# Performance work log

Hardware: AMD Instinct MI355X
Metric: run time of the kernel (lower is better)

The kernel has to match this reference:

```python
import jax, jax.numpy as jnp
import numpy as np

D_MODEL = 1024
N_HEADS = 16
HEAD_DIM = D_MODEL // N_HEADS
D_FF = 4096
LN_EPS = 1e-5


def setup_inputs() -> dict:
    key = jax.random.key(0)
    ks = jax.random.split(key, 13)
    s = lambda fan_in: 1.0 / np.sqrt(fan_in)
    return {
        "x": jax.random.normal(ks[0], (2, 2048, D_MODEL), dtype=jnp.float32),
        "w_qkv": jax.random.uniform(ks[1], (D_MODEL, 3 * D_MODEL), jnp.float32, -s(D_MODEL), s(D_MODEL)),
        "b_qkv": jax.random.uniform(ks[2], (3 * D_MODEL,), jnp.float32, -s(D_MODEL), s(D_MODEL)),
        "w_out": jax.random.uniform(ks[3], (D_MODEL, D_MODEL), jnp.float32, -s(D_MODEL), s(D_MODEL)),
        "b_out": jax.random.uniform(ks[4], (D_MODEL,), jnp.float32, -s(D_MODEL), s(D_MODEL)),
        "w_ff1": jax.random.uniform(ks[5], (D_MODEL, D_FF), jnp.float32, -s(D_MODEL), s(D_MODEL)),
        "b_ff1": jax.random.uniform(ks[6], (D_FF,), jnp.float32, -s(D_MODEL), s(D_MODEL)),
        "w_ff2": jax.random.uniform(ks[7], (D_FF, D_MODEL), jnp.float32, -s(D_FF), s(D_FF)),
        "b_ff2": jax.random.uniform(ks[8], (D_MODEL,), jnp.float32, -s(D_FF), s(D_FF)),
        "ln1_g": jnp.ones((D_MODEL,), jnp.float32),
        "ln1_b": jnp.zeros((D_MODEL,), jnp.float32),
        "ln2_g": jnp.ones((D_MODEL,), jnp.float32),
        "ln2_b": jnp.zeros((D_MODEL,), jnp.float32),
    }


def _layer_norm(x, g, b):
    mu = jnp.mean(x, axis=-1, keepdims=True)
    var = jnp.mean(jnp.square(x - mu), axis=-1, keepdims=True)
    return (x - mu) * jax.lax.rsqrt(var + LN_EPS) * g + b


def reference(x, w_qkv, b_qkv, w_out, b_out, w_ff1, b_ff1, w_ff2, b_ff2,
              ln1_g, ln1_b, ln2_g, ln2_b):
    B, S, D = x.shape
    scale = HEAD_DIM ** -0.5
    qkv = x @ w_qkv + b_qkv                                   # [B,S,3D]
    qkv = qkv.reshape(B, S, 3, N_HEADS, HEAD_DIM)
    q, k, v = (qkv[:, :, 0], qkv[:, :, 1], qkv[:, :, 2])      # [B,S,H,Dh]
    attn = jnp.einsum("bqhd,bkhd->bhqk", q, k) * scale        # [B,H,S,S]
    attn = jax.nn.softmax(attn, axis=-1)
    o = jnp.einsum("bhqk,bkhd->bqhd", attn, v).reshape(B, S, D)
    o = o @ w_out + b_out
    x = _layer_norm(x + o, ln1_g, ln1_b)
    # FFN: Linear -> exact GELU -> Linear (dropout = 0)
    h = jax.nn.gelu(x @ w_ff1 + b_ff1, approximate=False)
    ff = h @ w_ff2 + b_ff2
    x = _layer_norm(x + ff, ln2_g, ln2_b)
    return x
```

## Files before the change

kernel.cpp:

```cpp
#include <hip/hip_runtime.h>
#include <hip/hip_bf16.h>
#include <cstdint>
#include <cstddef>

using bf16 = __hip_bfloat16;
typedef __attribute__((ext_vector_type(8))) short bf16x8;
typedef __attribute__((ext_vector_type(4))) float f32x4;

#define TOKENS 4096
#define DMODEL 1024
#define DFF    4096
#define SEQ    2048
#define NHEAD  16
#define HDIM   64
#define KVBLK  64
#define NT     (SEQ / KVBLK)

__device__ __forceinline__ void async16(const void* g, void* l) {
  __builtin_amdgcn_global_load_lds(
      (const __attribute__((address_space(1))) void*)g,
      (__attribute__((address_space(3))) void*)l, 16, 0, 0);
}

__device__ __forceinline__ f32x4 mfma16(bf16x8 a, bf16x8 b, f32x4 c) {
  return __builtin_amdgcn_mfma_f32_16x16x32_bf16(a, b, c, 0, 0, 0);
}

__global__ void cast_bf16_k(const float* __restrict__ src, bf16* __restrict__ dst, int n) {
  int i = (blockIdx.x * blockDim.x + threadIdx.x) * 4;
  if (i >= n) return;
  float4 v = *(const float4*)(src + i);
  dst[i + 0] = __float2bfloat16(v.x);
  dst[i + 1] = __float2bfloat16(v.y);
  dst[i + 2] = __float2bfloat16(v.z);
  dst[i + 3] = __float2bfloat16(v.w);
}

__global__ void transpose_cast_k(const float* __restrict__ src, bf16* __restrict__ dst,
                                 int K, int N) {
  __shared__ float tile[32][33];
  int nt = blockIdx.x * 32, kt = blockIdx.y * 32;
  int tx = threadIdx.x, ty = threadIdx.y;
  #pragma unroll
  for (int i = 0; i < 32; i += 8)
    tile[ty + i][tx] = src[(size_t)(kt + ty + i) * N + nt + tx];
  __syncthreads();
  #pragma unroll
  for (int i = 0; i < 32; i += 8)
    dst[(size_t)(nt + ty + i) * K + kt + tx] = __float2bfloat16(tile[tx][ty + i]);
}

template <int EPI, int BN>
__global__ __launch_bounds__(256, 2)
void gemm_bt(const bf16* __restrict__ A, const bf16* __restrict__ Bt,
             const float* __restrict__ bias, int M, int N, int K,
             float* __restrict__ outf, bf16* __restrict__ outb,
             const float* __restrict__ resid,
             bf16* __restrict__ Qb, bf16* __restrict__ Kb, bf16* __restrict__ Vtb) {
  constexpr int MR = (BN == 128) ? 4 : 2;
  __shared__ bf16 Al[2][128 * 32];
  __shared__ bf16 Bl[2][BN * 32];
  const int t = threadIdx.x;
  const int nwg = gridDim.x * gridDim.y;
  const int flat = blockIdx.y * gridDim.x + blockIdx.x;
  const int swz = (flat & 7) * (nwg >> 3) + (flat >> 3);
  const int bm = (swz / gridDim.x) * 128, bn = (swz % gridDim.x) * BN;
  const int wid = t >> 6, lane = t & 63, g = lane >> 4, r = lane & 15;
  const int wr = (BN == 128) ? (wid >> 1) * 64 : wid * 32;
  const int wc = (BN == 128) ? (wid & 1) * 64 : 0;

  const f32x4 zero = {0.f, 0.f, 0.f, 0.f};
  f32x4 acc[MR][4];
  #pragma unroll
  for (int i = 0; i < MR; i++)
    #pragma unroll
    for (int j = 0; j < 4; j++) acc[i][j] = zero;

  const int ar0 = t >> 2, ac = (t & 3) * 8;
  const int ar1 = ar0 + 64;
  const int ach0 = t * 16, ach1 = ach0 + 4096;

  const int NK = K >> 5;
  #define STAGE(ktile, pb)                                                          \
    do {                                                                            \
      const int kk = (ktile) << 5;                                                  \
      async16(A + (size_t)(bm + ar0) * K + kk + ac, (char*)Al[pb] + ach0);          \
      async16(A + (size_t)(bm + ar1) * K + kk + ac, (char*)Al[pb] + ach1);          \
      async16(Bt + (size_t)(bn + ar0) * K + kk + ac, (char*)Bl[pb] + ach0);         \
      if constexpr (BN == 128)                                                      \
        async16(Bt + (size_t)(bn + ar1) * K + kk + ac, (char*)Bl[pb] + ach1);       \
    } while (0)

  STAGE(0, 0);
  asm volatile("s_waitcnt vmcnt(0)" ::: "memory");
  __builtin_amdgcn_s_barrier();

  #pragma unroll 1
  for (int it = 0; it < NK; ++it) {
    const int cur = it & 1;
    if (it + 1 < NK) STAGE(it + 1, cur ^ 1);
    bf16x8 af[MR], bfr[4];
    #pragma unroll
    for (int mt = 0; mt < MR; mt++)
      af[mt] = *(const bf16x8*)&Al[cur][(wr + mt * 16 + r) * 32 + 8 * g];
    #pragma unroll
    for (int nt = 0; nt < 4; nt++)
      bfr[nt] = *(const bf16x8*)&Bl[cur][(wc + nt * 16 + r) * 32 + 8 * g];
    #pragma unroll
    for (int mt = 0; mt < MR; mt++)
      #pragma unroll
      for (int nt = 0; nt < 4; nt++)
        acc[mt][nt] = mfma16(af[mt], bfr[nt], acc[mt][nt]);
    __builtin_amdgcn_sched_barrier(0);
    asm volatile("s_waitcnt vmcnt(0)" ::: "memory");
    __builtin_amdgcn_s_barrier();
  }
  #undef STAGE

  #pragma unroll
  for (int nt = 0; nt < 4; nt++) {
    const int col = bn + wc + nt * 16 + r;
    const float bv = bias[col];
    #pragma unroll
    for (int mt = 0; mt < MR; mt++) {
      #pragma unroll
      for (int j = 0; j < 4; j++) {
        const int row = bm + wr + mt * 16 + 4 * g + j;
        float v = acc[mt][nt][j] + bv;
        if constexpr (EPI == 0) {
          const int part = col >> 10, hd = col & 1023, h = hd >> 6, d = hd & 63;
          const int b_ = row >> 11, s_ = row & 2047;
          const bf16 q = __float2bfloat16(v);
          if (part == 0)      Qb[((size_t)(b_ * NHEAD + h) * SEQ + s_) * HDIM + d] = q;
          else if (part == 1) Kb[((size_t)(b_ * NHEAD + h) * SEQ + s_) * HDIM + d] = q;
          else                Vtb[((size_t)(b_ * NHEAD + h) * HDIM + d) * SEQ + s_] = q;
        } else if constexpr (EPI == 1) {
          const size_t idx = (size_t)row * N + col;
          outf[idx] = v + resid[idx];
        } else {
          const size_t idx = (size_t)row * N + col;
          outb[idx] = __float2bfloat16(0.5f * v * (1.f + erff(v * 0.70710678118f)));
        }
      }
    }
  }
}

__global__ __launch_bounds__(256, 4)
void attn_k(const bf16* __restrict__ Q, const bf16* __restrict__ Km,
            const bf16* __restrict__ Vt, bf16* __restrict__ O) {
  __shared__ bf16 Kl[2][KVBLK * 64];
  __shared__ bf16 Vl[2][KVBLK * 64];
  __shared__ bf16 P[4][16 * 64];
  const int b = blockIdx.x;
  const int bswz = (b & 7) * 128 + (b >> 3);
  const int bh = bswz >> 5, qb = bswz & 31;
  const int t = threadIdx.x, wid = t >> 6, lane = t & 63, g = lane >> 4, r = lane & 15;
  const int q0 = qb * 64 + wid * 16;
  const bf16* Qp = Q + (size_t)bh * SEQ * HDIM;
  const char* Kc = (const char*)(Km + (size_t)bh * SEQ * HDIM);
  const char* Vc = (const char*)(Vt + (size_t)bh * HDIM * SEQ);

  const bf16x8 qf0 = *(const bf16x8*)&Qp[(q0 + r) * HDIM + 8 * g];
  const bf16x8 qf1 = *(const bf16x8*)&Qp[(q0 + r) * HDIM + 8 * g + 32];

  const int o0 = wid * 2048 + lane * 16, o1 = o0 + 1024;
  const int cs0 = ((((o0 >> 4) & 7) ^ ((o0 >> 7) & 7)) << 4);
  const int cs1 = ((((o1 >> 4) & 7) ^ ((o1 >> 7) & 7)) << 4);
  const int kso0 = (o0 & ~127) + cs0, kso1 = (o1 & ~127) + cs1;
  const int vso0 = (o0 >> 7) * (SEQ * 2) + cs0, vso1 = (o1 >> 7) * (SEQ * 2) + cs1;

  const f32x4 zero = {0.f, 0.f, 0.f, 0.f};
  f32x4 oacc[4];
  #pragma unroll
  for (int i = 0; i < 4; i++) oacc[i] = zero;
  float mrow = -1e30f, lrow = 0.f;
  bf16* pl = P[wid];
  const int cA = ((g ^ (r & 7)) << 3), cB = (((g + 4) ^ (r & 7)) << 3);

  {
    const char* ks = Kc; const char* vs = Vc;
    char* kd = (char*)Kl[0]; char* vd = (char*)Vl[0];
    async16(ks + kso0, kd + o0); async16(ks + kso1, kd + o1);
    async16(vs + vso0, vd + o0); async16(vs + vso1, vd + o1);
  }

  #pragma unroll 1
  for (int tt = 0; tt < NT; ++tt) {
    if (tt + 1 < NT) {
      const char* ks = Kc + (tt + 1) * (KVBLK * HDIM * 2);
      const char* vs = Vc + (tt + 1) * (KVBLK * 2);
      char* kd = (char*)Kl[(tt + 1) & 1]; char* vd = (char*)Vl[(tt + 1) & 1];
      async16(ks + kso0, kd + o0); async16(ks + kso1, kd + o1);
      async16(vs + vso0, vd + o0); async16(vs + vso1, vd + o1);
      asm volatile("s_waitcnt vmcnt(4)" ::: "memory");
    } else {
      asm volatile("s_waitcnt vmcnt(0)" ::: "memory");
    }
    __builtin_amdgcn_sched_barrier(0);
    __builtin_amdgcn_s_barrier();
    __builtin_amdgcn_sched_barrier(0);

    const bf16* kbuf = Kl[tt & 1];
    const bf16* vbuf = Vl[tt & 1];

    f32x4 sacc[4];
    #pragma unroll
    for (int kt = 0; kt < 4; kt++) {
      const bf16* krow = kbuf + (kt * 16 + r) * 64;
      bf16x8 ka = *(const bf16x8*)&krow[cA];
      bf16x8 kb = *(const bf16x8*)&krow[cB];
      f32x4 s = zero;
      s = mfma16(ka, qf0, s);
      s = mfma16(kb, qf1, s);
      sacc[kt] = s;
    }

    float sv[4][4];
    #pragma unroll
    for (int kt = 0; kt < 4; kt++)
      #pragma unroll
      for (int j = 0; j < 4; j++) sv[kt][j] = sacc[kt][j] * 0.125f;
    float m0 = fmaxf(fmaxf(sv[0][0], sv[0][1]), fmaxf(sv[0][2], sv[0][3]));
    float m1 = fmaxf(fmaxf(sv[1][0], sv[1][1]), fmaxf(sv[1][2], sv[1][3]));
    float m2 = fmaxf(fmaxf(sv[2][0], sv[2][1]), fmaxf(sv[2][2], sv[2][3]));
    float m3 = fmaxf(fmaxf(sv[3][0], sv[3][1]), fmaxf(sv[3][2], sv[3][3]));
    float mx = fmaxf(fmaxf(m0, m1), fmaxf(m2, m3));
    mx = fmaxf(mx, __shfl_xor(mx, 16));
    mx = fmaxf(mx, __shfl_xor(mx, 32));
    const float mn = fmaxf(mrow, mx);
    const float corr = __expf(mrow - mn);
    mrow = mn;
    float sum = 0.f;
    #pragma unroll
    for (int kt = 0; kt < 4; kt++)
      #pragma unroll
      for (int j = 0; j < 4; j++) {
        const float p = __expf(sv[kt][j] - mn);
        sv[kt][j] = p;
        sum += p;
      }
    sum += __shfl_xor(sum, 16);
    sum += __shfl_xor(sum, 32);
    lrow = lrow * corr + sum;

    #pragma unroll
    for (int kt = 0; kt < 4; kt++) {
      bf16 pk[4] = {__float2bfloat16(sv[kt][0]), __float2bfloat16(sv[kt][1]),
                    __float2bfloat16(sv[kt][2]), __float2bfloat16(sv[kt][3])};
      const int pc = (((kt * 2 + (g >> 1)) ^ (r & 7)) << 4) + ((g & 1) << 3);
      *(short4*)((char*)pl + r * 128 + pc) = *(const short4*)pk;
    }
    asm volatile("s_waitcnt lgkmcnt(0)" ::: "memory");
    __builtin_amdgcn_sched_barrier(0);
    const bf16x8 pf0 = *(const bf16x8*)((const char*)pl + r * 128 + (cA << 1));
    const bf16x8 pf1 = *(const bf16x8*)((const char*)pl + r * 128 + (cB << 1));

    float cq[4];
    #pragma unroll
    for (int j = 0; j < 4; j++) cq[j] = __shfl(corr, 4 * g + j);

    #pragma unroll
    for (int dt = 0; dt < 4; dt++) {
      const bf16* vrow = vbuf + (dt * 16 + r) * 64;
      bf16x8 v0 = *(const bf16x8*)&vrow[cA];
      bf16x8 v1 = *(const bf16x8*)&vrow[cB];
      #pragma unroll
      for (int j = 0; j < 4; j++) oacc[dt][j] *= cq[j];
      oacc[dt] = mfma16(pf0, v0, oacc[dt]);
      oacc[dt] = mfma16(pf1, v1, oacc[dt]);
    }
    __builtin_amdgcn_sched_barrier(0);
    __builtin_amdgcn_s_barrier();
  }

  float lq[4];
  #pragma unroll
  for (int j = 0; j < 4; j++) lq[j] = __shfl(lrow, 4 * g + j);
  const int b_ = bh >> 4, h = bh & 15;
  #pragma unroll
  for (int dt = 0; dt < 4; dt++)
    #pragma unroll
    for (int j = 0; j < 4; j++) {
      const int tok = b_ * SEQ + q0 + 4 * g + j;
      O[(size_t)tok * DMODEL + h * HDIM + dt * 16 + r] =
          __float2bfloat16(oacc[dt][j] / lq[j]);
    }
}

__global__ __launch_bounds__(256)
void ln_k(const float* __restrict__ in, const float* __restrict__ gw,
          const float* __restrict__ bw, float* __restrict__ outf,
          bf16* __restrict__ outb) {
  const int row = blockIdx.x, t = threadIdx.x;
  const float4 v = *(const float4*)(in + (size_t)row * DMODEL + t * 4);
  float s = v.x + v.y + v.z + v.w;
  float s2 = v.x * v.x + v.y * v.y + v.z * v.z + v.w * v.w;
  #pragma unroll
  for (int m = 1; m < 64; m <<= 1) { s += __shfl_xor(s, m); s2 += __shfl_xor(s2, m); }
  __shared__ float red[8];
  const int wid = t >> 6, lane = t & 63;
  if (lane == 0) { red[wid] = s; red[4 + wid] = s2; }
  __syncthreads();
  s = red[0] + red[1] + red[2] + red[3];
  s2 = red[4] + red[5] + red[6] + red[7];
  const float mu = s * (1.f / DMODEL);
  const float rstd = rsqrtf(s2 * (1.f / DMODEL) - mu * mu + 1e-5f);
  const float4 gv = *(const float4*)(gw + t * 4);
  const float4 bv = *(const float4*)(bw + t * 4);
  float o0 = (v.x - mu) * rstd * gv.x + bv.x;
  float o1 = (v.y - mu) * rstd * gv.y + bv.y;
  float o2 = (v.z - mu) * rstd * gv.z + bv.z;
  float o3 = (v.w - mu) * rstd * gv.w + bv.w;
  if (outf) {
    float4 ov = {o0, o1, o2, o3};
    *(float4*)(outf + (size_t)row * DMODEL + t * 4) = ov;
  }
  if (outb) {
    bf16* p = outb + (size_t)row * DMODEL + t * 4;
    p[0] = __float2bfloat16(o0); p[1] = __float2bfloat16(o1);
    p[2] = __float2bfloat16(o2); p[3] = __float2bfloat16(o3);
  }
}

extern "C" void kernel_launch(void* const* d_in, const int* in_sizes, int n_in,
                              void* d_out, int out_size, void* d_ws, size_t ws_size,
                              hipStream_t stream) {
  const float* x     = (const float*)d_in[0];
  const float* w_qkv = (const float*)d_in[1];
  const float* b_qkv = (const float*)d_in[2];
  const float* w_out = (const float*)d_in[3];
  const float* b_out = (const float*)d_in[4];
  const float* w_ff1 = (const float*)d_in[5];
  const float* b_ff1 = (const float*)d_in[6];
  const float* w_ff2 = (const float*)d_in[7];
  const float* b_ff2 = (const float*)d_in[8];
  const float* ln1_g = (const float*)d_in[9];
  const float* ln1_b = (const float*)d_in[10];
  const float* ln2_g = (const float*)d_in[11];
  const float* ln2_b = (const float*)d_in[12];
  float* out = (float*)d_out;

  char* base = (char*)d_ws;
  bf16* wqkvT = (bf16*)(base);
  bf16* woutT = (bf16*)(base + 6291456);
  bf16* wff1T = (bf16*)(base + 8388608);
  bf16* wff2T = (bf16*)(base + 16777216);
  bf16* Qb    = (bf16*)(base + 25165824);
  bf16* Kb    = (bf16*)(base + 33554432);
  bf16* Vtb   = (bf16*)(base + 41943040);
  bf16* xob   = (bf16*)(base + 50331648);
  bf16* hb    = (bf16*)(base + 25165824);
  float* y    = (float*)(base + 58720256);
  float* x1f  = (float*)(base + 75497472);
  bf16* x1b   = (bf16*)(base + 92274688);
  (void)in_sizes; (void)n_in; (void)out_size; (void)ws_size;

  dim3 tb(32, 8);
  transpose_cast_k<<<dim3(3072 / 32, 1024 / 32), tb, 0, stream>>>(w_qkv, wqkvT, 1024, 3072);
  transpose_cast_k<<<dim3(1024 / 32, 1024 / 32), tb, 0, stream>>>(w_out, woutT, 1024, 1024);
  transpose_cast_k<<<dim3(4096 / 32, 1024 / 32), tb, 0, stream>>>(w_ff1, wff1T, 1024, 4096);
  transpose_cast_k<<<dim3(1024 / 32, 4096 / 32), tb, 0, stream>>>(w_ff2, wff2T, 4096, 1024);
  cast_bf16_k<<<(TOKENS * DMODEL / 4 + 255) / 256, 256, 0, stream>>>(x, xob, TOKENS * DMODEL);

  gemm_bt<0, 128><<<dim3(3072 / 128, TOKENS / 128), 256, 0, stream>>>(
      xob, wqkvT, b_qkv, TOKENS, 3072, 1024, nullptr, nullptr, nullptr, Qb, Kb, Vtb);
  attn_k<<<dim3(1024), 256, 0, stream>>>(Qb, Kb, Vtb, xob);
  gemm_bt<1, 64><<<dim3(1024 / 64, TOKENS / 128), 256, 0, stream>>>(
      xob, woutT, b_out, TOKENS, 1024, 1024, y, nullptr, x, nullptr, nullptr, nullptr);
  ln_k<<<TOKENS, 256, 0, stream>>>(y, ln1_g, ln1_b, x1f, x1b);
  gemm_bt<2, 128><<<dim3(4096 / 128, TOKENS / 128), 256, 0, stream>>>(
      x1b, wff1T, b_ff1, TOKENS, 4096, 1024, nullptr, hb, nullptr, nullptr, nullptr, nullptr);
  gemm_bt<1, 64><<<dim3(1024 / 64, TOKENS / 128), 256, 0, stream>>>(
      hb, wff2T, b_ff2, TOKENS, 1024, 4096, y, nullptr, x1f, nullptr, nullptr, nullptr);
  ln_k<<<TOKENS, 256, 0, stream>>>(y, ln2_g, ln2_b, out, nullptr);
}
```

Before: 290.7 us.

## Add 256x256 GEMM for QKV/FF1, fold softmax scale into Q, lazy rescale

Adds a new 512-thread GEMM kernel with 256x256 tiles, BK=64 and XOR-swizzled LDS, used for the QKV and FF1 projections. The QKV epilogue pre-scales Q by scale*log2(e) so attention can use exp2 directly. Attention now rescales the running max and output accumulator only when the new block max exceeds the old one by more than 8. s_setprio is wrapped around the MFMA sections in every kernel. The larger tiles increase register and LDS pressure and the wave count drops, and lazy rescaling relies on tolerating bounded exponent growth.

Result: slower. 315.5 us (+8.5%).

```diff
diff --git a/kernel.cpp b/kernel.cpp
--- a/kernel.cpp
+++ b/kernel.cpp
@@ -15,6 +15,7 @@
 #define HDIM   64
 #define KVBLK  64
 #define NT     (SEQ / KVBLK)
+#define QSCALE 0.1803368801111f
 
 __device__ __forceinline__ void async16(const void* g, void* l) {
   __builtin_amdgcn_global_load_lds(
@@ -48,6 +49,148 @@
   #pragma unroll
   for (int i = 0; i < 32; i += 8)
     dst[(size_t)(nt + ty + i) * K + kt + tx] = __float2bfloat16(tile[tx][ty + i]);
+}
+
+template <int EPI>
+__global__ __launch_bounds__(512, 2)
+void gemm256(const bf16* __restrict__ A, const bf16* __restrict__ Bt,
+             const float* __restrict__ bias, int M, int N, int K,
+             bf16* __restrict__ outb,
+             bf16* __restrict__ Qb, bf16* __restrict__ Kb, bf16* __restrict__ Vtb) {
+  __shared__ bf16 Al[2][256 * 64];
+  __shared__ bf16 Bl[2][256 * 64];
+  const int t = threadIdx.x;
+  const int nwg = gridDim.x * gridDim.y;
+  const int flat = blockIdx.y * gridDim.x + blockIdx.x;
+  const int swz = (flat & 7) * (nwg >> 3) + (flat >> 3);
+  const int bm = (swz / gridDim.x) * 256, bn = (swz % gridDim.x) * 256;
+  const int lane = t & 63, wid = t >> 6, g = lane >> 4, r = lane & 15;
+  const int wr = (wid >> 2) * 128, wc = (wid & 3) * 64;
+
+  const f32x4 zero = {0.f, 0.f, 0.f, 0.f};
+  f32x4 acc[8][4];
+  #pragma unroll
+  for (int i = 0; i < 8; i++)
+    #pragma unroll
+    for (int j = 0; j < 4; j++) acc[i][j] = zero;
+
+  const int srow = t >> 3, schunk = t & 7;
+  const int scol = ((schunk ^ (srow & 7)) << 3);
+
+  #define STAGE256(ktile, pb)                                             \
+    do {                                                                  \
+      const bf16* As = A + (size_t)(bm + srow) * K + (ktile) * 64 + scol; \
+      const bf16* Bs = Bt + (size_t)(bn + srow) * K + (ktile) * 64 + scol;\
+      char* Ad = (char*)Al[pb] + t * 16;                                  \
+      char* Bd = (char*)Bl[pb] + t * 16;                                  \
+      async16(As,            Ad);                                         \
+      async16(As + 64 * K,   Ad + 8192);                                  \
+      async16(As + 128 * K,  Ad + 16384);                                 \
+      async16(As + 192 * K,  Ad + 24576);                                 \
+      async16(Bs,            Bd);                                         \
+      async16(Bs + 64 * K,   Bd + 8192);                                  \
+      async16(Bs + 128 * K,  Bd + 16384);                                 \
+      async16(Bs + 192 * K,  Bd + 24576);                                 \
+    } while (0)
+
+  STAGE256(0, 0);
+  STAGE256(1, 1);
+  asm volatile("s_waitcnt vmcnt(8)" ::: "memory");
+  __builtin_amdgcn_sched_barrier(0);
+  __builtin_amdgcn_s_barrier();
+  __builtin_amdgcn_sched_barrier(0);
+
+  const int c0 = ((0 * 4 + g) ^ (r & 7)) << 4;
+  const int c1 = ((1 * 4 + g) ^ (r & 7)) << 4;
+
+  const int NK = K >> 6;
+  #pragma unroll 1
+  for (int tt = 0; tt < NK; ++tt) {
+    const int cur = tt & 1;
+    const char* Ab = (const char*)Al[cur];
+    const char* Bb = (const char*)Bl[cur];
+    bf16x8 bfr[4][2], af[4][2];
+    #pragma unroll
+    for (int nt = 0; nt < 4; nt++) {
+      const int rb = (wc + nt * 16 + r) * 128;
+      bfr[nt][0] = *(const bf16x8*)(Bb + rb + c0);
+      bfr[nt][1] = *(const bf16x8*)(Bb + rb + c1);
+    }
+    #pragma unroll
+    for (int mt = 0; mt < 4; mt++) {
+      const int rb = (wr + mt * 16 + r) * 128;
+      af[mt][0] = *(const bf16x8*)(Ab + rb + c0);
+      af[mt][1] = *(const bf16x8*)(Ab + rb + c1);
+    }
+    __builtin_amdgcn_s_setprio(1);
+    #pragma unroll
+    for (int mt = 0; mt < 4; mt++)
+      #pragma unroll
+      for (int nt = 0; nt < 4; nt++) {
+        acc[mt][nt] = mfma16(af[mt][0], bfr[nt][0], acc[mt][nt]);
+        acc[mt][nt] = mfma16(af[mt][1], bfr[nt][1], acc[mt][nt]);
+      }
+    __builtin_amdgcn_s_setprio(0);
+    #pragma unroll
+    for (int mt = 0; mt < 4; mt++) {
+      const int rb = (wr + 64 + mt * 16 + r) * 128;
+      af[mt][0] = *(const bf16x8*)(Ab + rb + c0);
+      af[mt][1] = *(const bf16x8*)(Ab + rb + c1);
+    }
+    __builtin_amdgcn_s_setprio(1);
+    #pragma unroll
+    for (int mt = 0; mt < 4; mt++)
+      #pragma unroll
+      for (int nt = 0; nt < 4; nt++) {
+        acc[4 + mt][nt] = mfma16(af[mt][0], bfr[nt][0], acc[4 + mt][nt]);
+        acc[4 + mt][nt] = mfma16(af[mt][1], bfr[nt][1], acc[4 + mt][nt]);
+      }
+    __builtin_amdgcn_s_setprio(0);
+    if (tt + 1 < NK) {
+      __builtin_amdgcn_sched_barrier(0);
+      __builtin_amdgcn_s_barrier();
+      __builtin_amdgcn_sched_barrier(0);
+      if (tt + 2 < NK) {
+        STAGE256(tt + 2, cur);
+        asm volatile("s_waitcnt vmcnt(8)" ::: "memory");
+      } else {
+        asm volatile("s_waitcnt vmcnt(0)" ::: "memory");
+      }
+      __builtin_amdgcn_sched_barrier(0);
+      __builtin_amdgcn_s_barrier();
+      __builtin_amdgcn_sched_barrier(0);
+    }
+  }
+  #undef STAGE256
+
+  #pragma unroll
+  for (int nt = 0; nt < 4; nt++) {
+    const int col = bn + wc + nt * 16 + r;
+    const float bv = bias[col];
+    #pragma unroll
+    for (int mt = 0; mt < 8; mt++) {
+      #pragma unroll
+      for (int j = 0; j < 4; j++) {
+        const int row = bm + wr + mt * 16 + 4 * g + j;
+        float v = acc[mt][nt][j] + bv;
+        if constexpr (EPI == 0) {
+          const int part = col >> 10, hd = col & 1023, h = hd >> 6, d = hd & 63;
+          const int b_ = row >> 11, s_ = row & 2047;
+          if (part == 0) {
+            Qb[((size_t)(b_ * NHEAD + h) * SEQ + s_) * HDIM + d] =
+                __float2bfloat16(v * QSCALE);
+          } else if (part == 1) {
+            Kb[((size_t)(b_ * NHEAD + h) * SEQ + s_) * HDIM + d] = __float2bfloat16(v);
+          } else {
+            Vtb[((size_t)(b_ * NHEAD + h) * HDIM + d) * SEQ + s_] = __float2bfloat16(v);
+          }
+        } else {
+          outb[(size_t)row * N + col] =
+              __float2bfloat16(0.5f * v * (1.f + erff(v * 0.70710678118f)));
+        }
+      }
+    }
+  }
 }
 
 template <int EPI, int BN>
@@ -106,11 +249,13 @@
     #pragma unroll
     for (int nt = 0; nt < 4; nt++)
       bfr[nt] = *(const bf16x8*)&Bl[cur][(wc + nt * 16 + r) * 32 + 8 * g];
+    __builtin_amdgcn_s_setprio(1);
     #pragma unroll
     for (int mt = 0; mt < MR; mt++)
       #pragma unroll
       for (int nt = 0; nt < 4; nt++)
         acc[mt][nt] = mfma16(af[mt], bfr[nt], acc[mt][nt]);
+    __builtin_amdgcn_s_setprio(0);
     __builtin_amdgcn_sched_barrier(0);
     asm volatile("s_waitcnt vmcnt(0)" ::: "memory");
     __builtin_amdgcn_s_barrier();
@@ -127,23 +272,12 @@
       for (int j = 0; j < 4; j++) {
         const int row = bm + wr + mt * 16 + 4 * g + j;
         float v = acc[mt][nt][j] + bv;
-        if constexpr (EPI == 0) {
-          const int part = col >> 10, hd = col & 1023, h = hd >> 6, d = hd & 63;
-          const int b_ = row >> 11, s_ = row & 2047;
-          const bf16 q = __float2bfloat16(v);
-          if (part == 0)      Qb[((size_t)(b_ * NHEAD + h) * SEQ + s_) * HDIM + d] = q;
-          else if (part == 1) Kb[((size_t)(b_ * NHEAD + h) * SEQ + s_) * HDIM + d] = q;
-          else                Vtb[((size_t)(b_ * NHEAD + h) * HDIM + d) * SEQ + s_] = q;
-        } else if constexpr (EPI == 1) {
-          const size_t idx = (size_t)row * N + col;
-          outf[idx] = v + resid[idx];
-        } else {
-          const size_t idx = (size_t)row * N + col;
-          outb[idx] = __float2bfloat16(0.5f * v * (1.f + erff(v * 0.70710678118f)));
-        }
+        const size_t idx = (size_t)row * N + col;
+        outf[idx] = v + resid[idx];
       }
     }
   }
+  (void)outb; (void)Qb; (void)Kb; (void)Vtb;
 }
 
 __global__ __launch_bounds__(256, 4)
@@ -179,10 +313,9 @@
   const int cA = ((g ^ (r & 7)) << 3), cB = (((g + 4) ^ (r & 7)) << 3);
 
   {
-    const char* ks = Kc; const char* vs = Vc;
     char* kd = (char*)Kl[0]; char* vd = (char*)Vl[0];
-    async16(ks + kso0, kd + o0); async16(ks + kso1, kd + o1);
-    async16(vs + vso0, vd + o0); async16(vs + vso1, vd + o1);
+    async16(Kc + kso0, kd + o0); async16(Kc + kso1, kd + o1);
+    async16(Vc + vso0, vd + o0); async16(Vc + vso1, vd + o1);
   }
 
   #pragma unroll 1
@@ -205,6 +338,7 @@
     const bf16* vbuf = Vl[tt & 1];
 
     f32x4 sacc[4];
+    __builtin_amdgcn_s_setprio(1);
     #pragma unroll
     for (int kt = 0; kt < 4; kt++) {
       const bf16* krow = kbuf + (kt * 16 + r) * 64;
@@ -215,28 +349,29 @@
       s = mfma16(kb, qf1, s);
       sacc[kt] = s;
     }
-
-    float sv[4][4];
-    #pragma unroll
-    for (int kt = 0; kt < 4; kt++)
-      #pragma unroll
-      for (int j = 0; j < 4; j++) sv[kt][j] = sacc[kt][j] * 0.125f;
-    float m0 = fmaxf(fmaxf(sv[0][0], sv[0][1]), fmaxf(sv[0][2], sv[0][3]));
-    float m1 = fmaxf(fmaxf(sv[1][0], sv[1][1]), fmaxf(sv[1][2], sv[1][3]));
-    float m2 = fmaxf(fmaxf(sv[2][0], sv[2][1]), fmaxf(sv[2][2], sv[2][3]));
-    float m3 = fmaxf(fmaxf(sv[3][0], sv[3][1]), fmaxf(sv[3][2], sv[3][3]));
+    __builtin_amdgcn_s_setprio(0);
+
+    float m0 = fmaxf(fmaxf(sacc[0][0], sacc[0][1]), fmaxf(sacc[0][2], sacc[0][3]));
+    float m1 = fmaxf(fmaxf(sacc[1][0], sacc[1][1]), fmaxf(sacc[1][2], sacc[1][3]));
+    float m2 = fmaxf(fmaxf(sacc[2][0], sacc[2][1]), fmaxf(sacc[2][2], sacc[2][3]));
+    float m3 = fmaxf(fmaxf(sacc[3][0], sacc[3][1]), fmaxf(sacc[3][2], sacc[3][3]));
     float mx = fmaxf(fmaxf(m0, m1), fmaxf(m2, m3));
     mx = fmaxf(mx, __shfl_xor(mx, 16));
     mx = fmaxf(mx, __shfl_xor(mx, 32));
-    const float mn = fmaxf(mrow, mx);
-    const float corr = __expf(mrow - mn);
-    mrow = mn;
+    const bool grow = !__all(mx <= mrow + 8.f);
+    float corr = 1.f;
+    if (grow) {
+      const float mn = fmaxf(mrow, mx);
+      corr = exp2f(mrow - mn);
+      mrow = mn;
+    }
     float sum = 0.f;
+    float sv[4][4];
     #pragma unroll
     for (int kt = 0; kt < 4; kt++)
       #pragma unroll
       for (int j = 0; j < 4; j++) {
-        const float p = __expf(sv[kt][j] - mn);
+        const float p = exp2f(sacc[kt][j] - mrow);
         sv[kt][j] = p;
         sum += p;
       }
@@ -256,20 +391,26 @@
     const bf16x8 pf0 = *(const bf16x8*)((const char*)pl + r * 128 + (cA << 1));
     const bf16x8 pf1 = *(const bf16x8*)((const char*)pl + r * 128 + (cB << 1));
 
-    float cq[4];
-    #pragma unroll
-    for (int j = 0; j < 4; j++) cq[j] = __shfl(corr, 4 * g + j);
-
+    if (grow) {
+      float cq[4];
+      #pragma unroll
+      for (int j = 0; j < 4; j++) cq[j] = __shfl(corr, 4 * g + j);
+      #pragma unroll
+      for (int dt = 0; dt < 4; dt++)
+        #pragma unroll
+        for (int j = 0; j < 4; j++) oacc[dt][j] *= cq[j];
+    }
+
+    __builtin_amdgcn_s_setprio(1);
     #pragma unroll
     for (int dt = 0; dt < 4; dt++) {
       const bf16* vrow = vbuf + (dt * 16 + r) * 64;
       bf16x8 v0 = *(const bf16x8*)&vrow[cA];
       bf16x8 v1 = *(const bf16x8*)&vrow[cB];
-      #pragma unroll
-      for (int j = 0; j < 4; j++) oacc[dt][j] *= cq[j];
       oacc[dt] = mfma16(pf0, v0, oacc[dt]);
       oacc[dt] = mfma16(pf1, v1, oacc[dt]);
     }
+    __builtin_amdgcn_s_setprio(0);
     __builtin_amdgcn_sched_barrier(0);
     __builtin_amdgcn_s_barrier();
   }
@@ -363,14 +504,14 @@
   transpose_cast_k<<<dim3(1024 / 32, 4096 / 32), tb, 0, stream>>>(w_ff2, wff2T, 4096, 1024);
   cast_bf16_k<<<(TOKENS * DMODEL / 4 + 255) / 256, 256, 0, stream>>>(x, xob, TOKENS * DMODEL);
 
-  gemm_bt<0, 128><<<dim3(3072 / 128, TOKENS / 128), 256, 0, stream>>>(
-      xob, wqkvT, b_qkv, TOKENS, 3072, 1024, nullptr, nullptr, nullptr, Qb, Kb, Vtb);
+  gemm256<0><<<dim3(3072 / 256, TOKENS / 256), 512, 0, stream>>>(
+      xob, wqkvT, b_qkv, TOKENS, 3072, 1024, nullptr, Qb, Kb, Vtb);
   attn_k<<<dim3(1024), 256, 0, stream>>>(Qb, Kb, Vtb, xob);
   gemm_bt<1, 64><<<dim3(1024 / 64, TOKENS / 128), 256, 0, stream>>>(
       xob, woutT, b_out, TOKENS, 1024, 1024, y, nullptr, x, nullptr, nullptr, nullptr);
   ln_k<<<TOKENS, 256, 0, stream>>>(y, ln1_g, ln1_b, x1f, x1b);
-  gemm_bt<2, 128><<<dim3(4096 / 128, TOKENS / 128), 256, 0, stream>>>(
-      x1b, wff1T, b_ff1, TOKENS, 4096, 1024, nullptr, hb, nullptr, nullptr, nullptr, nullptr);
+  gemm256<2><<<dim3(4096 / 256, TOKENS / 256), 512, 0, stream>>>(
+      x1b, wff1T, b_ff1, TOKENS, 4096, 1024, hb, nullptr, nullptr, nullptr);
   gemm_bt<1, 64><<<dim3(1024 / 64, TOKENS / 128), 256, 0, stream>>>(
       hb, wff2T, b_ff2, TOKENS, 1024, 4096, y, nullptr, x1f, nullptr, nullptr, nullptr);
   ln_k<<<TOKENS, 256, 0, stream>>>(y, ln2_g, ln2_b, out, nullptr);
```

## Triple-buffer GEMM loads, fold softmax scale into Q, use exp2 with lazy rescale

Applied to the files above, without the earlier changes.

The GEMM moves from double to triple buffering in LDS. It issues loads two tiles ahead, waits on a partial vmcnt, and raises wave priority around the MFMA block to hide global-load latency. In attention, the QKV epilogue pre-scales Q by scale*log2(e) so softmax can call the raw v_exp_f32 (exp2) without a per-element multiply. The running-max update and output rescale are skipped unless some row's max grows by more than 8 (log2 units), which cuts shuffles and multiplies per KV tile. The costs are more LDS per GEMM workgroup, which may lower occupancy, and small numerical drift from the threshold rescaling.

Result: slower. 304.3 us (+4.7%).

```diff
diff --git a/kernel.cpp b/kernel.cpp
--- a/kernel.cpp
+++ b/kernel.cpp
@@ -15,6 +15,7 @@
 #define HDIM   64
 #define KVBLK  64
 #define NT     (SEQ / KVBLK)
+#define QSCALE 0.1803368801111f
 
 __device__ __forceinline__ void async16(const void* g, void* l) {
   __builtin_amdgcn_global_load_lds(
@@ -24,6 +25,12 @@
 
 __device__ __forceinline__ f32x4 mfma16(bf16x8 a, bf16x8 b, f32x4 c) {
   return __builtin_amdgcn_mfma_f32_16x16x32_bf16(a, b, c, 0, 0, 0);
+}
+
+__device__ __forceinline__ float exp2_fast(float x) {
+  float r;
+  asm("v_exp_f32 %0, %1" : "=v"(r) : "v"(x));
+  return r;
 }
 
 __global__ void cast_bf16_k(const float* __restrict__ src, bf16* __restrict__ dst, int n) {
@@ -58,8 +65,8 @@
              const float* __restrict__ resid,
              bf16* __restrict__ Qb, bf16* __restrict__ Kb, bf16* __restrict__ Vtb) {
   constexpr int MR = (BN == 128) ? 4 : 2;
-  __shared__ bf16 Al[2][128 * 32];
-  __shared__ bf16 Bl[2][BN * 32];
+  __shared__ bf16 Al[3][128 * 32];
+  __shared__ bf16 Bl[3][BN * 32];
   const int t = threadIdx.x;
   const int nwg = gridDim.x * gridDim.y;
   const int flat = blockIdx.y * gridDim.x + blockIdx.x;
@@ -92,13 +99,24 @@
     } while (0)
 
   STAGE(0, 0);
-  asm volatile("s_waitcnt vmcnt(0)" ::: "memory");
-  __builtin_amdgcn_s_barrier();
-
+  STAGE(1, 1);
+
+  int cur = 0, stg = 2;
   #pragma unroll 1
   for (int it = 0; it < NK; ++it) {
-    const int cur = it & 1;
-    if (it + 1 < NK) STAGE(it + 1, cur ^ 1);
+    if (it + 1 < NK) {
+      if constexpr (BN == 128)
+        asm volatile("s_waitcnt vmcnt(4)" ::: "memory");
+      else
+        asm volatile("s_waitcnt vmcnt(3)" ::: "memory");
+    } else {
+      asm volatile("s_waitcnt vmcnt(0)" ::: "memory");
+    }
+    __builtin_amdgcn_sched_barrier(0);
+    __builtin_amdgcn_s_barrier();
+    __builtin_amdgcn_sched_barrier(0);
+    if (it + 2 < NK) STAGE(it + 2, stg);
+
     bf16x8 af[MR], bfr[4];
     #pragma unroll
     for (int mt = 0; mt < MR; mt++)
@@ -106,14 +124,15 @@
     #pragma unroll
     for (int nt = 0; nt < 4; nt++)
       bfr[nt] = *(const bf16x8*)&Bl[cur][(wc + nt * 16 + r) * 32 + 8 * g];
+    __builtin_amdgcn_s_setprio(1);
     #pragma unroll
     for (int mt = 0; mt < MR; mt++)
       #pragma unroll
       for (int nt = 0; nt < 4; nt++)
         acc[mt][nt] = mfma16(af[mt], bfr[nt], acc[mt][nt]);
-    __builtin_amdgcn_sched_barrier(0);
-    asm volatile("s_waitcnt vmcnt(0)" ::: "memory");
-    __builtin_amdgcn_s_barrier();
+    __builtin_amdgcn_s_setprio(0);
+    cur = (cur == 2) ? 0 : cur + 1;
+    stg = (stg == 2) ? 0 : stg + 1;
   }
   #undef STAGE
 
@@ -130,10 +149,14 @@
         if constexpr (EPI == 0) {
           const int part = col >> 10, hd = col & 1023, h = hd >> 6, d = hd & 63;
           const int b_ = row >> 11, s_ = row & 2047;
-          const bf16 q = __float2bfloat16(v);
-          if (part == 0)      Qb[((size_t)(b_ * NHEAD + h) * SEQ + s_) * HDIM + d] = q;
-          else if (part == 1) Kb[((size_t)(b_ * NHEAD + h) * SEQ + s_) * HDIM + d] = q;
-          else                Vtb[((size_t)(b_ * NHEAD + h) * HDIM + d) * SEQ + s_] = q;
+          if (part == 0) {
+            Qb[((size_t)(b_ * NHEAD + h) * SEQ + s_) * HDIM + d] =
+                __float2bfloat16(v * QSCALE);
+          } else if (part == 1) {
+            Kb[((size_t)(b_ * NHEAD + h) * SEQ + s_) * HDIM + d] = __float2bfloat16(v);
+          } else {
+            Vtb[((size_t)(b_ * NHEAD + h) * HDIM + d) * SEQ + s_] = __float2bfloat16(v);
+          }
         } else if constexpr (EPI == 1) {
           const size_t idx = (size_t)row * N + col;
           outf[idx] = v + resid[idx];
@@ -179,10 +202,9 @@
   const int cA = ((g ^ (r & 7)) << 3), cB = (((g + 4) ^ (r & 7)) << 3);
 
   {
-    const char* ks = Kc; const char* vs = Vc;
     char* kd = (char*)Kl[0]; char* vd = (char*)Vl[0];
-    async16(ks + kso0, kd + o0); async16(ks + kso1, kd + o1);
-    async16(vs + vso0, vd + o0); async16(vs + vso1, vd + o1);
+    async16(Kc + kso0, kd + o0); async16(Kc + kso1, kd + o1);
+    async16(Vc + vso0, vd + o0); async16(Vc + vso1, vd + o1);
   }
 
   #pragma unroll 1
@@ -216,27 +238,27 @@
       sacc[kt] = s;
     }
 
-    float sv[4][4];
-    #pragma unroll
-    for (int kt = 0; kt < 4; kt++)
-      #pragma unroll
-      for (int j = 0; j < 4; j++) sv[kt][j] = sacc[kt][j] * 0.125f;
-    float m0 = fmaxf(fmaxf(sv[0][0], sv[0][1]), fmaxf(sv[0][2], sv[0][3]));
-    float m1 = fmaxf(fmaxf(sv[1][0], sv[1][1]), fmaxf(sv[1][2], sv[1][3]));
-    float m2 = fmaxf(fmaxf(sv[2][0], sv[2][1]), fmaxf(sv[2][2], sv[2][3]));
-    float m3 = fmaxf(fmaxf(sv[3][0], sv[3][1]), fmaxf(sv[3][2], sv[3][3]));
+    float m0 = fmaxf(fmaxf(sacc[0][0], sacc[0][1]), fmaxf(sacc[0][2], sacc[0][3]));
+    float m1 = fmaxf(fmaxf(sacc[1][0], sacc[1][1]), fmaxf(sacc[1][2], sacc[1][3]));
+    float m2 = fmaxf(fmaxf(sacc[2][0], sacc[2][1]), fmaxf(sacc[2][2], sacc[2][3]));
+    float m3 = fmaxf(fmaxf(sacc[3][0], sacc[3][1]), fmaxf(sacc[3][2], sacc[3][3]));
     float mx = fmaxf(fmaxf(m0, m1), fmaxf(m2, m3));
     mx = fmaxf(mx, __shfl_xor(mx, 16));
     mx = fmaxf(mx, __shfl_xor(mx, 32));
-    const float mn = fmaxf(mrow, mx);
-    const float corr = __expf(mrow - mn);
-    mrow = mn;
+    const bool grow = !__all(mx <= mrow + 8.f);
+    float corr = 1.f;
+    if (grow) {
+      const float mn = fmaxf(mrow, mx);
+      corr = exp2_fast(mrow - mn);
+      mrow = mn;
+    }
     float sum = 0.f;
+    float sv[4][4];
     #pragma unroll
     for (int kt = 0; kt < 4; kt++)
       #pragma unroll
       for (int j = 0; j < 4; j++) {
-        const float p = __expf(sv[kt][j] - mn);
+        const float p = exp2_fast(sacc[kt][j] - mrow);
         sv[kt][j] = p;
         sum += p;
       }
@@ -256,17 +278,21 @@
     const bf16x8 pf0 = *(const bf16x8*)((const char*)pl + r * 128 + (cA << 1));
     const bf16x8 pf1 = *(const bf16x8*)((const char*)pl + r * 128 + (cB << 1));
 
-    float cq[4];
-    #pragma unroll
-    for (int j = 0; j < 4; j++) cq[j] = __shfl(corr, 4 * g + j);
+    if (grow) {
+      float cq[4];
+      #pragma unroll
+      for (int j = 0; j < 4; j++) cq[j] = __shfl(corr, 4 * g + j);
+      #pragma unroll
+      for (int dt = 0; dt < 4; dt++)
+        #pragma unroll
+        for (int j = 0; j < 4; j++) oacc[dt][j] *= cq[j];
+    }
 
     #pragma unroll
     for (int dt = 0; dt < 4; dt++) {
       const bf16* vrow = vbuf + (dt * 16 + r) * 64;
       bf16x8 v0 = *(const bf16x8*)&vrow[cA];
       bf16x8 v1 = *(const bf16x8*)&vrow[cB];
-      #pragma unroll
-      for (int j = 0; j < 4; j++) oacc[dt][j] *= cq[j];
       oacc[dt] = mfma16(pf0, v0, oacc[dt]);
       oacc[dt] = mfma16(pf1, v1, oacc[dt]);
     }
```
